# Performance work log

Hardware: AMD Instinct MI355X
Metric: run time of the kernel (lower is better)

Reference implementation:

```python
import jax, jax.numpy as jnp
import numpy as np

EPS = 1e-5


def spmm(rows, cols, vals, x):
    # x: (B, C, V); y[b,c,v] = sum_{e: rows[e]==v} vals[e] * x[b,c,cols[e]]
    B, C, V = x.shape
    xt = x.reshape(B * C, V).T                      # (V, B*C)
    msg = vals[:, None] * xt[cols]                  # (E, B*C)
    y = jax.ops.segment_sum(msg, rows, num_segments=V)
    return y.T.reshape(B, C, V)


def cheb_conv(x, W, b, rows, cols, vals):
    # W: (K, Cin, Cout); Chebyshev recurrence over node dim
    K = W.shape[0]
    Tk = [x]
    if K > 1:
        Tk.append(spmm(rows, cols, vals, x))
    for _ in range(2, K):
        Tk.append(2.0 * spmm(rows, cols, vals, Tk[-1]) - Tk[-2])
    T = jnp.stack(Tk)                               # (K, B, Cin, V)
    out = jnp.einsum('kbiv,kio->bov', T, W)
    if b is not None:
        out = out + b[None, :, None]
    return out


def bn(x, g, be):
    # BatchNorm1d training-mode stats over (batch, nodes) per channel
    m = jnp.mean(x, axis=(0, 2), keepdims=True)
    v = jnp.var(x, axis=(0, 2), keepdims=True)
    return (x - m) * jax.lax.rsqrt(v + EPS) * g[None, :, None] + be[None, :, None]


def res_block(x, rows, cols, vals, ga, bea, Wa, ba, gb, beb, Wb, bb, Ws=None):
    xn = bn(x, ga, bea)
    out = cheb_conv(xn, Wa, ba, rows, cols, vals)
    out = bn(jax.nn.relu(out), gb, beb)
    out = cheb_conv(out, Wb, bb, rows, cols, vals)
    sc = xn if Ws is None else cheb_conv(xn, Ws, None, rows, cols, vals)
    return jax.nn.relu(out + sc)


def setup_inputs() -> dict:
    key = jax.random.key(0)
    ks = iter(jax.random.split(key, 40))
    V, E, B, K = 50000, 800000, 8, 4
    d = {}
    d['x'] = jax.random.normal(next(ks), (B, 16, V), dtype=jnp.float32)
    d['lap_rows'] = jax.random.randint(next(ks), (E,), 0, V, dtype=jnp.int32)
    d['lap_cols'] = jax.random.randint(next(ks), (E,), 0, V, dtype=jnp.int32)
    d['lap_vals'] = jax.random.normal(next(ks), (E,), dtype=jnp.float32) * 0.05

    def w(shape, scale=0.1):
        return jax.random.normal(next(ks), shape, dtype=jnp.float32) * scale

    d['W_in'], d['b_in'] = w((K, 16, 32)), w((32,))
    # block 1: 32 -> [32] -> 32 (identity shortcut)
    d['g1a'], d['be1a'] = jnp.ones(32), jnp.zeros(32)
    d['W1a'], d['b1a'] = w((K, 32, 32)), w((32,))
    d['g1b'], d['be1b'] = jnp.ones(32), jnp.zeros(32)
    d['W1b'], d['b1b'] = w((K, 32, 32)), w((32,))
    # block 2: 32 -> [64] -> 64 (ChebConv K=1 shortcut, no bias)
    d['g2a'], d['be2a'] = jnp.ones(32), jnp.zeros(32)
    d['W2a'], d['b2a'] = w((K, 32, 64)), w((64,))
    d['g2b'], d['be2b'] = jnp.ones(64), jnp.zeros(64)
    d['W2b'], d['b2b'] = w((K, 64, 64)), w((64,))
    d['W2s'] = w((1, 32, 64))
    # block 3: 64 -> [64] -> 64 (identity shortcut)
    d['g3a'], d['be3a'] = jnp.ones(64), jnp.zeros(64)
    d['W3a'], d['b3a'] = w((K, 64, 64)), w((64,))
    d['g3b'], d['be3b'] = jnp.ones(64), jnp.zeros(64)
    d['W3b'], d['b3b'] = w((K, 64, 64)), w((64,))
    # output head
    d['g_out'], d['be_out'] = jnp.ones(64), jnp.zeros(64)
    d['W_out'], d['b_out'] = w((K, 64, 10)), w((10,))
    return d


def reference(x, lap_rows, lap_cols, lap_vals,
              W_in, b_in,
              g1a, be1a, W1a, b1a, g1b, be1b, W1b, b1b,
              g2a, be2a, W2a, b2a, g2b, be2b, W2b, b2b, W2s,
              g3a, be3a, W3a, b3a, g3b, be3b, W3b, b3b,
              g_out, be_out, W_out, b_out):
    r, c, v = lap_rows, lap_cols, lap_vals
    out = jax.nn.relu(cheb_conv(x, W_in, b_in, r, c, v))
    out = res_block(out, r, c, v, g1a, be1a, W1a, b1a, g1b, be1b, W1b, b1b)
    out = res_block(out, r, c, v, g2a, be2a, W2a, b2a, g2b, be2b, W2b, b2b, W2s)
    out = res_block(out, r, c, v, g3a, be3a, W3a, b3a, g3b, be3b, W3b, b3b)
    out = bn(out, g_out, be_out)
    out = jax.nn.relu(cheb_conv(out, W_out, b_out, r, c, v))
    pooled = jnp.max(out, axis=2)                   # global max pool over nodes -> (B, 10)
    return jax.nn.log_softmax(pooled, axis=1)
```

## Files before the change

kernel.cpp:

```cpp
#include <hip/hip_runtime.h>
#include <hip/hip_bf16.h>
#include <hip/hip_fp16.h>

typedef float v2f __attribute__((ext_vector_type(2)));
__device__ __forceinline__ v2f vfma2(v2f a, v2f b, v2f c) {
#if __has_builtin(__builtin_elementwise_fma)
    return __builtin_elementwise_fma(a, b, c);
#else
    v2f d; d.x = fmaf(a.x, b.x, c.x); d.y = fmaf(a.y, b.y, c.y); return d;
#endif
}

__global__ void hist_kernel(const int* __restrict__ rows, int* __restrict__ counts, int E) {
    int i = blockIdx.x * blockDim.x + threadIdx.x;
    if (i < E) atomicAdd(&counts[rows[i]], 1);
}

__global__ void chunk_sum_kernel(const int* __restrict__ counts, int* __restrict__ chunk_sums, int V) {
    __shared__ int sh[256];
    int t = threadIdx.x;
    int i = blockIdx.x * 256 + t;
    sh[t] = (i < V) ? counts[i] : 0;
    __syncthreads();
    for (int st = 128; st > 0; st >>= 1) {
        if (t < st) sh[t] += sh[t + st];
        __syncthreads();
    }
    if (t == 0) chunk_sums[blockIdx.x] = sh[0];
}

__global__ void scan_chunks_kernel(int* __restrict__ cs, int n) {
    __shared__ int wsum[4];
    int t = threadIdx.x, lane = t & 63, w = t >> 6;
    int orig = (t < n) ? cs[t] : 0;
    int x = orig;
    #pragma unroll
    for (int d = 1; d < 64; d <<= 1) {
        int y = __shfl_up(x, d);
        if (lane >= d) x += y;
    }
    if (lane == 63) wsum[w] = x;
    __syncthreads();
    int wo = 0;
    for (int j = 0; j < w; ++j) wo += wsum[j];
    if (t < n) cs[t] = wo + x - orig;
}

__global__ void scan_final_kernel(const int* __restrict__ counts, const int* __restrict__ chunk_off,
                                  int* __restrict__ row_ptr, int V) {
    __shared__ int wsum[4];
    int t = threadIdx.x, lane = t & 63, w = t >> 6;
    int i = blockIdx.x * 256 + t;
    int x = (i < V) ? counts[i] : 0;
    #pragma unroll
    for (int d = 1; d < 64; d <<= 1) {
        int y = __shfl_up(x, d);
        if (lane >= d) x += y;
    }
    if (lane == 63) wsum[w] = x;
    __syncthreads();
    int wo = 0;
    for (int j = 0; j < w; ++j) wo += wsum[j];
    if (i < V) row_ptr[i + 1] = chunk_off[blockIdx.x] + wo + x;
    if (i == 0) row_ptr[0] = 0;
}

__global__ void init_cursor_kernel(const int* __restrict__ row_ptr, int* __restrict__ cursor, int V) {
    int i = blockIdx.x * blockDim.x + threadIdx.x;
    if (i < V) cursor[i] = row_ptr[i];
}

__global__ void scatter_kernel(const int* __restrict__ rows, const int* __restrict__ cols,
                               const float* __restrict__ vals, int* __restrict__ cursor,
                               int* __restrict__ cols_s, float* __restrict__ vals_s, int E) {
    int i = blockIdx.x * blockDim.x + threadIdx.x;
    if (i < E) {
        int r = rows[i];
        int p = atomicAdd(&cursor[r], 1);
        cols_s[p] = cols[i];
        vals_s[p] = vals[i];
    }
}

__global__ void sort_rows_kernel(const int* __restrict__ row_ptr, int* cols, float* vals, int V) {
    int v = blockIdx.x * blockDim.x + threadIdx.x;
    if (v >= V) return;
    int e0 = row_ptr[v], e1 = row_ptr[v + 1];
    for (int i = e0 + 1; i < e1; ++i) {
        int c = cols[i];
        unsigned xb = __float_as_uint(vals[i]);
        int j = i - 1;
        while (j >= e0) {
            int cj = cols[j];
            unsigned vj = __float_as_uint(vals[j]);
            if (cj > c || (cj == c && vj > xb)) {
                cols[j + 1] = cj; vals[j + 1] = __uint_as_float(vj);
                --j;
            } else break;
        }
        cols[j + 1] = c;
        vals[j + 1] = __uint_as_float(xb);
    }
}

__global__ void transpose_in_kernel(const float* __restrict__ x, __half* __restrict__ X, int V) {
    int total = V * 128;
    for (int i = blockIdx.x * blockDim.x + threadIdx.x; i < total; i += gridDim.x * blockDim.x) {
        int v = i >> 7;
        int t = i & 127;
        X[i] = __float2half(x[t * V + v]);
    }
}

template <int VPT> struct PackT;
template <> struct PackT<1> { using T = float;  };
template <> struct PackT<2> { using T = float2; };
template <> struct PackT<4> { using T = float4; };

template <int VPT>
__global__ __launch_bounds__(256) void spmm2_kernel(
    const int* __restrict__ row_ptr, const int* __restrict__ cols,
    const float* __restrict__ vals, const __half2* __restrict__ src,
    __half2* dst, const __half2* prev, int V) {
    using T = typename PackT<VPT>::T;
    union U { T raw; __half2 h[VPT]; };
    int lane = threadIdx.x & 63;
    int v = (blockIdx.x << 2) | (threadIdx.x >> 6);
    if (v >= V) return;
    const int W = VPT * 64;
    const size_t row = (size_t)v * W + lane * VPT;

    float pr[2 * VPT];
    bool hasp = (prev != nullptr);
    if (hasp) {
        U pv; pv.raw = *(const T*)(prev + row);
        #pragma unroll
        for (int j = 0; j < VPT; ++j) {
            float2 f = __half22float2(pv.h[j]);
            pr[2 * j] = f.x; pr[2 * j + 1] = f.y;
        }
    }
    float acc[2 * VPT];
    #pragma unroll
    for (int j = 0; j < 2 * VPT; ++j) acc[j] = 0.f;

    int e0 = row_ptr[v], e1 = row_ptr[v + 1];
    int e = e0;
    for (; e + 8 <= e1; e += 8) {
        int   c[8]; float w[8]; U g[8];
        #pragma unroll
        for (int k = 0; k < 8; ++k) { c[k] = cols[e + k]; w[k] = vals[e + k]; }
        #pragma unroll
        for (int k = 0; k < 8; ++k)
            g[k].raw = *(const T*)(src + (size_t)c[k] * W + lane * VPT);
        #pragma unroll
        for (int k = 0; k < 8; ++k) {
            #pragma unroll
            for (int j = 0; j < VPT; ++j) {
                float2 f = __half22float2(g[k].h[j]);
                acc[2*j] += w[k] * f.x; acc[2*j+1] += w[k] * f.y;
            }
        }
    }
    for (; e + 4 <= e1; e += 4) {
        int   c[4]; float w[4]; U g[4];
        #pragma unroll
        for (int k = 0; k < 4; ++k) { c[k] = cols[e + k]; w[k] = vals[e + k]; }
        #pragma unroll
        for (int k = 0; k < 4; ++k)
            g[k].raw = *(const T*)(src + (size_t)c[k] * W + lane * VPT);
        #pragma unroll
        for (int k = 0; k < 4; ++k) {
            #pragma unroll
            for (int j = 0; j < VPT; ++j) {
                float2 f = __half22float2(g[k].h[j]);
                acc[2*j] += w[k] * f.x; acc[2*j+1] += w[k] * f.y;
            }
        }
    }
    for (; e < e1; ++e) {
        int c = cols[e]; float wv = vals[e];
        U g; g.raw = *(const T*)(src + (size_t)c * W + lane * VPT);
        #pragma unroll
        for (int j = 0; j < VPT; ++j) {
            float2 f = __half22float2(g.h[j]);
            acc[2*j] += wv * f.x; acc[2*j+1] += wv * f.y;
        }
    }
    if (hasp) {
        #pragma unroll
        for (int j = 0; j < 2 * VPT; ++j) acc[j] = 2.f * acc[j] - pr[j];
    }
    U o;
    #pragma unroll
    for (int j = 0; j < VPT; ++j) o.h[j] = __floats2half2_rn(acc[2*j], acc[2*j+1]);
    *(T*)(dst + row) = o.raw;
}

template <int CIN, int COUT>
__global__ __launch_bounds__(256) void combine_kernel(
    const __half* T0, const __half* T1, const __half* T2, const __half* T3,
    const float* __restrict__ W, const float* __restrict__ bias,
    const __half* res, const __half* sc, const float* __restrict__ Wsc,
    __half* out, int relu, int V) {
    constexpr int SL    = CIN / 8;
    constexpr int BURST = (SL < 4) ? SL : 4;
    constexpr int NB    = SL / BURST;
    constexpr int SLS   = 32 / 8;
    union U4 { float4 raw; __half2 h[4]; };
    union UW { float4 raw; v2f p[2]; };

    int g = blockIdx.x * 256 + threadIdx.x;
    if (g >= V * 8) return;

    v2f acc[COUT / 2];
    #pragma unroll
    for (int c = 0; c < COUT / 2; ++c) {
        if (bias) { acc[c].x = bias[2 * c]; acc[c].y = bias[2 * c + 1]; }
        else      { acc[c].x = 0.f;         acc[c].y = 0.f; }
    }

    auto rank1 = [&](float2 a, const float* w0f, const float* w1f) {
        v2f ax = {a.x, a.x}, ay = {a.y, a.y};
        if constexpr (COUT % 4 == 0) {
            const float4* w0 = (const float4*)w0f;
            const float4* w1 = (const float4*)w1f;
            #pragma unroll
            for (int cw = 0; cw < COUT / 4; ++cw) {
                UW A; A.raw = w0[cw];
                UW B; B.raw = w1[cw];
                acc[2 * cw]     = vfma2(ax, A.p[0], acc[2 * cw]);
                acc[2 * cw]     = vfma2(ay, B.p[0], acc[2 * cw]);
                acc[2 * cw + 1] = vfma2(ax, A.p[1], acc[2 * cw + 1]);
                acc[2 * cw + 1] = vfma2(ay, B.p[1], acc[2 * cw + 1]);
            }
        } else {
            const v2f* w0 = (const v2f*)w0f;
            const v2f* w1 = (const v2f*)w1f;
            #pragma unroll
            for (int c = 0; c < COUT / 2; ++c) {
                acc[c] = vfma2(ax, w0[c], acc[c]);
                acc[c] = vfma2(ay, w1[c], acc[c]);
            }
        }
    };

    const __half* Ts[4] = {T0, T1, T2, T3};
    #pragma unroll 1
    for (int k = 0; k < 4; ++k) {
        const float4* rp = (const float4*)(Ts[k] + (size_t)g * CIN);
        const float* Wk = W + (size_t)k * CIN * COUT;
        #pragma unroll 1
        for (int b2 = 0; b2 < NB; ++b2) {
            U4 x[BURST];
            #pragma unroll
            for (int j = 0; j < BURST; ++j) x[j].raw = rp[b2 * BURST + j];
            #pragma unroll
            for (int j = 0; j < BURST; ++j) {
                #pragma unroll
                for (int s = 0; s < 4; ++s) {
                    int q = (b2 * BURST + j) * 4 + s;
                    float2 a = __half22float2(x[j].h[s]);
                    rank1(a, Wk + (size_t)(2 * q) * COUT,
                             Wk + (size_t)(2 * q + 1) * COUT);
                }
            }
        }
    }
    if (sc) {
        const float4* sp = (const float4*)(sc + (size_t)g * 32);
        U4 x[SLS];
        #pragma unroll
        for (int j = 0; j < SLS; ++j) x[j].raw = sp[j];
        #pragma unroll
        for (int j = 0; j < SLS; ++j) {
            #pragma unroll
            for (int s = 0; s < 4; ++s) {
                int q = j * 4 + s;
                float2 a = __half22float2(x[j].h[s]);
                rank1(a, Wsc + (size_t)(2 * q) * COUT,
                         Wsc + (size_t)(2 * q + 1) * COUT);
            }
        }
    }

    size_t ob = (size_t)g * COUT;
    if constexpr (COUT % 8 == 0) {
        if (res) {
            const float4* rr = (const float4*)(res + ob);
            #pragma unroll
            for (int q = 0; q < COUT / 8; ++q) {
                U4 rv; rv.raw = rr[q];
                #pragma unroll
                for (int s = 0; s < 4; ++s) {
                    float2 f = __half22float2(rv.h[s]);
                    acc[q * 4 + s].x += f.x; acc[q * 4 + s].y += f.y;
                }
            }
        }
        if (relu) {
            #pragma unroll
            for (int c = 0; c < COUT / 2; ++c) {
                acc[c].x = fmaxf(acc[c].x, 0.f);
                acc[c].y = fmaxf(acc[c].y, 0.f);
            }
        }
        float4* ro = (float4*)(out + ob);
        #pragma unroll
        for (int q = 0; q < COUT / 8; ++q) {
            U4 o;
            #pragma unroll
            for (int s = 0; s < 4; ++s)
                o.h[s] = __floats2half2_rn(acc[q * 4 + s].x, acc[q * 4 + s].y);
            ro[q] = o.raw;
        }
    } else {
        if (res) {
            const __half2* rr = (const __half2*)(res + ob);
            #pragma unroll
            for (int c = 0; c < COUT / 2; ++c) {
                float2 f = __half22float2(rr[c]);
                acc[c].x += f.x; acc[c].y += f.y;
            }
        }
        if (relu) {
            #pragma unroll
            for (int c = 0; c < COUT / 2; ++c) {
                acc[c].x = fmaxf(acc[c].x, 0.f);
                acc[c].y = fmaxf(acc[c].y, 0.f);
            }
        }
        __half2* ro = (__half2*)(out + ob);
        #pragma unroll
        for (int c = 0; c < COUT / 2; ++c)
            ro[c] = __floats2half2_rn(acc[c].x, acc[c].y);
    }
}

__global__ void bn_stats_part_kernel(const __half2* __restrict__ x2, int C, int relu_in,
                                     float* __restrict__ part, size_t N2) {
    __shared__ float sx[256], qx[256], sy[256], qy[256];
    int t = threadIdx.x;
    size_t i0 = (size_t)blockIdx.x * 256 + t;
    size_t step = (size_t)gridDim.x * 256;
    float ax = 0.f, aqx = 0.f, ay = 0.f, aqy = 0.f;
    for (size_t i = i0; i < N2; i += step) {
        float2 f = __half22float2(x2[i]);
        if (relu_in) { f.x = fmaxf(f.x, 0.f); f.y = fmaxf(f.y, 0.f); }
        ax += f.x; aqx += f.x * f.x;
        ay += f.y; aqy += f.y * f.y;
    }
    sx[t] = ax; qx[t] = aqx; sy[t] = ay; qy[t] = aqy;
    __syncthreads();
    int half = C >> 1;
    for (int st = 128; st >= half; st >>= 1) {
        if (t < st) {
            sx[t] += sx[t + st]; qx[t] += qx[t + st];
            sy[t] += sy[t + st]; qy[t] += qy[t + st];
        }
        __syncthreads();
    }
    if (t < half) {
        part[blockIdx.x * 128 + 2 * t]         = sx[t];
        part[blockIdx.x * 128 + 2 * t + 1]     = sy[t];
        part[blockIdx.x * 128 + C + 2 * t]     = qx[t];
        part[blockIdx.x * 128 + C + 2 * t + 1] = qy[t];
    }
}

__global__ void bn_reduce_kernel(const float* __restrict__ part, int nblk,
                                 const float* __restrict__ g, const float* __restrict__ be,
                                 float* __restrict__ ss, int C, float invN) {
    int c = threadIdx.x;
    if (c < C) {
        float s = 0.f, q = 0.f;
        for (int b = 0; b < nblk; ++b) {
            s += part[b * 128 + c];
            q += part[b * 128 + C + c];
        }
        float m = s * invN;
        float var = q * invN - m * m;
        float sc = g[c] * rsqrtf(var + 1e-5f);
        ss[c] = sc;
        ss[C + c] = be[c] - m * sc;
    }
}

__global__ void affine_h_kernel(__half* x, const float* __restrict__ ss, int C,
                                int relu_in, size_t N2) {
    union U4 { float4 raw; __half2 h[4]; };
    size_t NG = N2 >> 2;
    size_t stride = (size_t)gridDim.x * blockDim.x;
    size_t i0 = (size_t)blockIdx.x * blockDim.x + threadIdx.x;
    float4* x4 = (float4*)x;
    int c0 = (int)((8 * i0) & (size_t)(C - 1));
    float sc[8], of[8];
    #pragma unroll
    for (int j = 0; j < 8; ++j) { sc[j] = ss[c0 + j]; of[j] = ss[C + c0 + j]; }
    for (size_t i = i0; i < NG; i += stride) {
        U4 u; u.raw = x4[i];
        #pragma unroll
        for (int j = 0; j < 4; ++j) {
            float2 f = __half22float2(u.h[j]);
            if (relu_in) { f.x = fmaxf(f.x, 0.f); f.y = fmaxf(f.y, 0.f); }
            f.x = f.x * sc[2 * j] + of[2 * j];
            f.y = f.y * sc[2 * j + 1] + of[2 * j + 1];
            u.h[j] = __floats2half2_rn(f.x, f.y);
        }
        x4[i] = u.raw;
    }
}

__global__ void maxpool_h_kernel(const __half* __restrict__ x, float* pooled, int V, int NS) {
    __shared__ float red[256];
    int o = blockIdx.x % 80;
    int slice = blockIdx.x / 80;
    int v0 = (int)((long long)V * slice / NS);
    int v1 = (int)((long long)V * (slice + 1) / NS);
    float m = 0.f;
    for (int v = v0 + threadIdx.x; v < v1; v += 256)
        m = fmaxf(m, __half2float(x[(size_t)v * 80 + o]));
    red[threadIdx.x] = m;
    __syncthreads();
    for (int st = 128; st > 0; st >>= 1) {
        if (threadIdx.x < st) red[threadIdx.x] = fmaxf(red[threadIdx.x], red[threadIdx.x + st]);
        __syncthreads();
    }
    if (threadIdx.x == 0) atomicMax((int*)&pooled[o], __float_as_int(red[0]));
}

__global__ void lsm_kernel(const float* __restrict__ pooled, float* __restrict__ out) {
    int b = threadIdx.x;
    if (b < 8) {
        float m = -1e30f;
        for (int c = 0; c < 10; ++c) m = fmaxf(m, pooled[b * 10 + c]);
        float s = 0.f;
        for (int c = 0; c < 10; ++c) s += expf(pooled[b * 10 + c] - m);
        float l = logf(s);
        for (int c = 0; c < 10; ++c)
            out[b * 10 + c] = pooled[b * 10 + c] - m - l;
    }
}

__global__ void encode_kernel(float* out, float val) {
    int i = threadIdx.x;
    if (i < 80) out[i] = val;
}

extern "C" void kernel_launch(void* const* d_in, const int* in_sizes, int n_in,
                              void* d_out, int out_size, void* d_ws, size_t ws_size,
                              hipStream_t stream) {
    (void)in_sizes; (void)n_in; (void)out_size;
    const int V = 50000, E = 800000;
    const int NCH = (V + 255) / 256;
    const int SB = 512;
    const int NS = 8;

    auto al = [](size_t x) { return (x + 255) & ~(size_t)255; };
    const size_t FB = al((size_t)V * 512 * sizeof(__half));
    const size_t need = 5 * FB + al((V + 1) * 4) + al(V * 4) + al(E * 4) + al(E * 4)
                      + al((size_t)SB * 128 * 4) + al(8 * 128 * 4) + al(80 * 4) + al(NCH * 4);
    if (ws_size < need) {
        encode_kernel<<<1, 128, 0, stream>>>((float*)d_out, (float)(ws_size >> 20));
        return;
    }

    const float* x_in = (const float*)d_in[0];
    const int* rows   = (const int*)d_in[1];
    const int* colsi  = (const int*)d_in[2];
    const float* lvals = (const float*)d_in[3];
    const float* W_in = (const float*)d_in[4];
    const float* b_in = (const float*)d_in[5];
    const float* g1a = (const float*)d_in[6],  *be1a = (const float*)d_in[7];
    const float* W1a = (const float*)d_in[8],  *b1a  = (const float*)d_in[9];
    const float* g1b = (const float*)d_in[10], *be1b = (const float*)d_in[11];
    const float* W1b = (const float*)d_in[12], *b1b  = (const float*)d_in[13];
    const float* g2a = (const float*)d_in[14], *be2a = (const float*)d_in[15];
    const float* W2a = (const float*)d_in[16], *b2a  = (const float*)d_in[17];
    const float* g2b = (const float*)d_in[18], *be2b = (const float*)d_in[19];
    const float* W2b = (const float*)d_in[20], *b2b  = (const float*)d_in[21];
    const float* W2s = (const float*)d_in[22];
    const float* g3a = (const float*)d_in[23], *be3a = (const float*)d_in[24];
    const float* W3a = (const float*)d_in[25], *b3a  = (const float*)d_in[26];
    const float* g3b = (const float*)d_in[27], *be3b = (const float*)d_in[28];
    const float* W3b = (const float*)d_in[29], *b3b  = (const float*)d_in[30];
    const float* g_o = (const float*)d_in[31], *be_o = (const float*)d_in[32];
    const float* W_o = (const float*)d_in[33], *b_o  = (const float*)d_in[34];

    char* wp = (char*)d_ws;
    auto take = [&](size_t bytes) -> void* { void* p = (void*)wp; wp += al(bytes); return p; };
    __half* P0 = (__half*)take(FB);
    __half* P1 = (__half*)take(FB);
    __half* P2 = (__half*)take(FB);
    __half* P3 = (__half*)take(FB);
    __half* P4 = (__half*)take(FB);
    int* row_ptr  = (int*)take((V + 1) * sizeof(int));
    int* cursor   = (int*)take(V * sizeof(int));
    int* cols_s   = (int*)take(E * sizeof(int));
    float* vals_s = (float*)take(E * sizeof(float));
    float* part   = (float*)take((size_t)SB * 128 * sizeof(float));
    float* aff    = (float*)take(8 * 128 * sizeof(float));
    float* pooled = (float*)take(80 * sizeof(float));
    int* chunks   = (int*)take(NCH * sizeof(int));

    hipMemsetAsync(cursor, 0, V * sizeof(int), stream);
    hipMemsetAsync(pooled, 0, 80 * sizeof(float), stream);

    hist_kernel<<<(E + 255) / 256, 256, 0, stream>>>(rows, cursor, E);
    chunk_sum_kernel<<<NCH, 256, 0, stream>>>(cursor, chunks, V);
    scan_chunks_kernel<<<1, 256, 0, stream>>>(chunks, NCH);
    scan_final_kernel<<<NCH, 256, 0, stream>>>(cursor, chunks, row_ptr, V);
    init_cursor_kernel<<<(V + 255) / 256, 256, 0, stream>>>(row_ptr, cursor, V);
    scatter_kernel<<<(E + 255) / 256, 256, 0, stream>>>(rows, colsi, lvals, cursor, cols_s, vals_s, E);
    sort_rows_kernel<<<(V + 255) / 256, 256, 0, stream>>>(row_ptr, cols_s, vals_s, V);
    transpose_in_kernel<<<4096, 256, 0, stream>>>(x_in, P0, V);

    const int SG = (V + 3) / 4;
    auto spmm = [&](const __half* src, __half* dst, const __half* prev, int C) {
        if (C == 16)
            spmm2_kernel<1><<<SG, 256, 0, stream>>>(row_ptr, cols_s, vals_s,
                (const __half2*)src, (__half2*)dst, (const __half2*)prev, V);
        else if (C == 32)
            spmm2_kernel<2><<<SG, 256, 0, stream>>>(row_ptr, cols_s, vals_s,
                (const __half2*)src, (__half2*)dst, (const __half2*)prev, V);
        else
            spmm2_kernel<4><<<SG, 256, 0, stream>>>(row_ptr, cols_s, vals_s,
                (const __half2*)src, (__half2*)dst, (const __half2*)prev, V);
    };
    auto cheb3 = [&](const __half* a, __half* b, __half* c, __half* d, int C) {
        spmm(a, b, nullptr, C);
        spmm(b, c, a, C);
        spmm(c, d, b, C);
    };
    const int MG = (V * 8 + 255) / 256;
    auto comb = [&](const __half* T0, const __half* T1, const __half* T2, const __half* T3,
                    int Cin, int Cout, const float* W, const float* bias,
                    const __half* res, const __half* sc, const float* Wsc,
                    __half* out, int relu) {
        if (Cin == 16 && Cout == 32)
            combine_kernel<16, 32><<<MG, 256, 0, stream>>>(T0, T1, T2, T3, W, bias, res, sc, Wsc, out, relu, V);
        else if (Cin == 32 && Cout == 32)
            combine_kernel<32, 32><<<MG, 256, 0, stream>>>(T0, T1, T2, T3, W, bias, res, sc, Wsc, out, relu, V);
        else if (Cin == 32 && Cout == 64)
            combine_kernel<32, 64><<<MG, 256, 0, stream>>>(T0, T1, T2, T3, W, bias, res, sc, Wsc, out, relu, V);
        else if (Cin == 64 && Cout == 64)
            combine_kernel<64, 64><<<MG, 256, 0, stream>>>(T0, T1, T2, T3, W, bias, res, sc, Wsc, out, relu, V);
        else
            combine_kernel<64, 10><<<MG, 256, 0, stream>>>(T0, T1, T2, T3, W, bias, res, sc, Wsc, out, relu, V);
    };
    auto stats = [&](const __half* xb, int C, int relu, int slot, const float* g, const float* be) {
        bn_stats_part_kernel<<<SB, 256, 0, stream>>>((const __half2*)xb, C, relu, part,
                                                     (size_t)V * 4 * C);
        bn_reduce_kernel<<<1, 64, 0, stream>>>(part, SB, g, be, aff + slot * 128, C,
                                               1.f / ((float)V * 8.f));
    };
    auto affine = [&](__half* xb, int C, int relu, int slot) {
        affine_h_kernel<<<2048, 256, 0, stream>>>(xb, aff + slot * 128, C, relu,
                                                  (size_t)V * 4 * C);
    };
    const __half* NH = nullptr;
    const float*  NF = nullptr;

    cheb3(P0, P1, P2, P3, 16);
    comb(P0, P1, P2, P3, 16, 32, W_in, b_in, NH, NH, NF, P4, 1);

    stats(P4, 32, 0, 0, g1a, be1a);
    affine(P4, 32, 0, 0);
    cheb3(P4, P0, P1, P2, 32);
    comb(P4, P0, P1, P2, 32, 32, W1a, b1a, NH, NH, NF, P0, 0);
    stats(P0, 32, 1, 1, g1b, be1b);
    affine(P0, 32, 1, 1);
    cheb3(P0, P1, P2, P3, 32);
    comb(P0, P1, P2, P3, 32, 32, W1b, b1b, P4, NH, NF, P4, 1);

    stats(P4, 32, 0, 2, g2a, be2a);
    affine(P4, 32, 0, 2);
    cheb3(P4, P0, P1, P2, 32);
    comb(P4, P0, P1, P2, 32, 64, W2a, b2a, NH, NH, NF, P3, 0);
    stats(P3, 64, 1, 3, g2b, be2b);
    affine(P3, 64, 1, 3);
    cheb3(P3, P0, P1, P2, 64);
    comb(P3, P0, P1, P2, 64, 64, W2b, b2b, NH, P4, W2s, P0, 1);

    stats(P0, 64, 0, 4, g3a, be3a);
    affine(P0, 64, 0, 4);
    cheb3(P0, P1, P2, P3, 64);
    comb(P0, P1, P2, P3, 64, 64, W3a, b3a, NH, NH, NF, P1, 0);
    stats(P1, 64, 1, 5, g3b, be3b);
    affine(P1, 64, 1, 5);
    cheb3(P1, P2, P3, P4, 64);
    comb(P1, P2, P3, P4, 64, 64, W3b, b3b, P0, NH, NF, P1, 1);

    stats(P1, 64, 0, 6, g_o, be_o);
    affine(P1, 64, 0, 6);
    cheb3(P1, P0, P2, P3, 64);
    comb(P1, P0, P2, P3, 64, 10, W_o, b_o, NH, NH, NF, P4, 1);
    maxpool_h_kernel<<<80 * NS, 256, 0, stream>>>(P4, pooled, V, NS);
    lsm_kernel<<<1, 64, 0, stream>>>(pooled, (float*)d_out);
}
```

Before: 4.471 ms.

## Use split-fp16 MFMA for 64-channel Chebyshev combine

Replaces the scalar FMA combine kernel for the 64->64 layers with a matrix-core kernel using 16x16x32 f16 MFMA. Weights are split into high and low fp16 halves so their precision stays close to fp32, and a small prep kernel transposes them per call. The aim is to cut the ALU cost of the dense channel-mixing step. It costs extra weight-prep launches, doubled MFMA work, and direct scalar output stores that may not coalesce well. The diff does not show whether the optional shortcut path's 32 input channels line up with how the shortcut is actually used.

```diff
diff --git a/kernel.cpp b/kernel.cpp
--- a/kernel.cpp
+++ b/kernel.cpp
@@ -10,6 +10,9 @@
     v2f d; d.x = fmaf(a.x, b.x, c.x); d.y = fmaf(a.y, b.y, c.y); return d;
 #endif
 }
+
+typedef _Float16 half8v __attribute__((ext_vector_type(8)));
+typedef float    f32x4  __attribute__((ext_vector_type(4)));
 
 __global__ void hist_kernel(const int* __restrict__ rows, int* __restrict__ counts, int E) {
     int i = blockIdx.x * blockDim.x + threadIdx.x;
@@ -197,6 +200,75 @@
     *(T*)(dst + row) = o.raw;
 }
 
+__global__ void wprep_kernel(const float* __restrict__ W, __half* __restrict__ Bh,
+                             __half* __restrict__ Bl, int KT) {
+    int i = blockIdx.x * 256 + threadIdx.x;
+    if (i >= KT * 64) return;
+    int kt = i >> 6, co = i & 63;
+    float w = W[(size_t)kt * 64 + co];
+    __half h = __float2half_rn(w);
+    Bh[(size_t)co * KT + kt] = h;
+    Bl[(size_t)co * KT + kt] = __float2half_rn(w - __half2float(h));
+}
+
+__global__ __launch_bounds__(256) void combine64_mfma_kernel(
+    const __half* T0, const __half* T1, const __half* T2, const __half* T3,
+    const __half* __restrict__ Bh, const __half* __restrict__ Bl,
+    const float* __restrict__ bias,
+    const __half* res, const __half* sc,
+    const __half* __restrict__ Bsh, const __half* __restrict__ Bsl,
+    __half* out, int relu, int V) {
+    int l   = threadIdx.x & 63;
+    int wid = threadIdx.x >> 6;
+    int row0 = blockIdx.x * 64 + wid * 16;
+    if (row0 >= V * 8) return;
+    int lr = l & 15, lg = l >> 4;
+
+    f32x4 acc[4];
+    #pragma unroll
+    for (int ct = 0; ct < 4; ++ct) {
+        float b = bias ? bias[ct * 16 + lr] : 0.f;
+        acc[ct] = (f32x4){b, b, b, b};
+    }
+
+    const __half* Ts[4] = {T0, T1, T2, T3};
+    #pragma unroll
+    for (int s = 0; s < 8; ++s) {
+        const __half* ap = Ts[s >> 1] + (size_t)(row0 + lr) * 64 + (s & 1) * 32 + lg * 8;
+        half8v a = *(const half8v*)ap;
+        #pragma unroll
+        for (int ct = 0; ct < 4; ++ct) {
+            half8v bh = *(const half8v*)(Bh + (size_t)(ct * 16 + lr) * 256 + s * 32 + lg * 8);
+            half8v bl = *(const half8v*)(Bl + (size_t)(ct * 16 + lr) * 256 + s * 32 + lg * 8);
+            acc[ct] = __builtin_amdgcn_mfma_f32_16x16x32_f16(a, bh, acc[ct], 0, 0, 0);
+            acc[ct] = __builtin_amdgcn_mfma_f32_16x16x32_f16(a, bl, acc[ct], 0, 0, 0);
+        }
+    }
+    if (sc) {
+        half8v a2 = *(const half8v*)(sc + (size_t)(row0 + lr) * 32 + lg * 8);
+        #pragma unroll
+        for (int ct = 0; ct < 4; ++ct) {
+            half8v bh = *(const half8v*)(Bsh + (size_t)(ct * 16 + lr) * 32 + lg * 8);
+            half8v bl = *(const half8v*)(Bsl + (size_t)(ct * 16 + lr) * 32 + lg * 8);
+            acc[ct] = __builtin_amdgcn_mfma_f32_16x16x32_f16(a2, bh, acc[ct], 0, 0, 0);
+            acc[ct] = __builtin_amdgcn_mfma_f32_16x16x32_f16(a2, bl, acc[ct], 0, 0, 0);
+        }
+    }
+
+    #pragma unroll
+    for (int ct = 0; ct < 4; ++ct) {
+        #pragma unroll
+        for (int j = 0; j < 4; ++j) {
+            int r = row0 + lg * 4 + j;
+            int c = ct * 16 + lr;
+            float v = acc[ct][j];
+            if (res) v += __half2float(res[(size_t)r * 64 + c]);
+            if (relu) v = fmaxf(v, 0.f);
+            out[(size_t)r * 64 + c] = __float2half_rn(v);
+        }
+    }
+}
+
 template <int CIN, int COUT>
 __global__ __launch_bounds__(256) void combine_kernel(
     const __half* T0, const __half* T1, const __half* T2, const __half* T3,
@@ -458,8 +530,10 @@
 
     auto al = [](size_t x) { return (x + 255) & ~(size_t)255; };
     const size_t FB = al((size_t)V * 512 * sizeof(__half));
+    const size_t WPB = al((size_t)256 * 64 * 2) * 2 + al((size_t)32 * 64 * 2) * 2;
     const size_t need = 5 * FB + al((V + 1) * 4) + al(V * 4) + al(E * 4) + al(E * 4)
-                      + al((size_t)SB * 128 * 4) + al(8 * 128 * 4) + al(80 * 4) + al(NCH * 4);
+                      + al((size_t)SB * 128 * 4) + al(8 * 128 * 4) + al(80 * 4) + al(NCH * 4)
+                      + WPB;
     if (ws_size < need) {
         encode_kernel<<<1, 128, 0, stream>>>((float*)d_out, (float)(ws_size >> 20));
         return;
@@ -502,6 +576,10 @@
     float* aff    = (float*)take(8 * 128 * sizeof(float));
     float* pooled = (float*)take(80 * sizeof(float));
     int* chunks   = (int*)take(NCH * sizeof(int));
+    __half* wbh   = (__half*)take((size_t)256 * 64 * 2);
+    __half* wbl   = (__half*)take((size_t)256 * 64 * 2);
+    __half* wsh   = (__half*)take((size_t)32 * 64 * 2);
+    __half* wsl   = (__half*)take((size_t)32 * 64 * 2);
 
     hipMemsetAsync(cursor, 0, V * sizeof(int), stream);
     hipMemsetAsync(pooled, 0, 80 * sizeof(float), stream);
@@ -537,14 +615,17 @@
                     int Cin, int Cout, const float* W, const float* bias,
                     const __half* res, const __half* sc, const float* Wsc,
                     __half* out, int relu) {
-        if (Cin == 16 && Cout == 32)
+        if (Cin == 64 && Cout == 64) {
+            wprep_kernel<<<(256 * 64 + 255) / 256, 256, 0, stream>>>(W, wbh, wbl, 256);
+            if (sc) wprep_kernel<<<(32 * 64 + 255) / 256, 256, 0, stream>>>(Wsc, wsh, wsl, 32);
+            combine64_mfma_kernel<<<(V * 8) / 64, 256, 0, stream>>>(
+                T0, T1, T2, T3, wbh, wbl, bias, res, sc, wsh, wsl, out, relu, V);
+        } else if (Cin == 16 && Cout == 32)
             combine_kernel<16, 32><<<MG, 256, 0, stream>>>(T0, T1, T2, T3, W, bias, res, sc, Wsc, out, relu, V);
         else if (Cin == 32 && Cout == 32)
             combine_kernel<32, 32><<<MG, 256, 0, stream>>>(T0, T1, T2, T3, W, bias, res, sc, Wsc, out, relu, V);
         else if (Cin == 32 && Cout == 64)
             combine_kernel<32, 64><<<MG, 256, 0, stream>>>(T0, T1, T2, T3, W, bias, res, sc, Wsc, out, relu, V);
-        else if (Cin == 64 && Cout == 64)
-            combine_kernel<64, 64><<<MG, 256, 0, stream>>>(T0, T1, T2, T3, W, bias, res, sc, Wsc, out, relu, V);
         else
             combine_kernel<64, 10><<<MG, 256, 0, stream>>>(T0, T1, T2, T3, W, bias, res, sc, Wsc, out, relu, V);
     };
```

New measurement: 4.473 ms. About the same (+0.1%).
